# Performance work log

Measured on AMD Instinct MI355X. Metric: run time of the kernel, lower is better.

The kernel has to match this reference:

```python
import jax, jax.numpy as jnp
import numpy as np

N, IN_DIM, NUM_HEADS, HEAD_DIM = 8192, 256, 4, 64
NEG_SLOPE = 0.2


def setup_inputs() -> dict:
    key = jax.random.key(0)
    k1, k2, k3, k4 = jax.random.split(key, 4)
    h = jax.random.normal(k1, (N, IN_DIM), dtype=jnp.float32)
    adj = jax.random.randint(k2, (N, N), 0, 2, dtype=jnp.int32)
    # xavier-ish init scale for the per-head projection weights and attention vector
    W = jax.random.normal(k3, (NUM_HEADS, IN_DIM, HEAD_DIM), dtype=jnp.float32) * (1.0 / np.sqrt(IN_DIM))
    a = jax.random.normal(k4, (2 * HEAD_DIM, 1), dtype=jnp.float32) * (1.0 / np.sqrt(2 * HEAD_DIM))
    return {"h": h, "adj": adj, "W": W, "a": a}


def reference(h, adj, W, a):
    # Wh: (H, N, D) -- per-head linear projection (no bias)
    Wh = jnp.einsum('ni,hid->hnd', h, W)
    # torch computes cat([Wh_i, Wh_j]) @ a; equivalent decomposition:
    # e_ij = (Wh_i . a[:D]) + (Wh_j . a[D:])  -- avoids the O(N^2 * 2D) concat tensor
    a1 = a[:HEAD_DIM, 0]  # (D,)
    a2 = a[HEAD_DIM:, 0]  # (D,)
    s_i = jnp.einsum('hnd,d->hn', Wh, a1)  # (H, N)
    s_j = jnp.einsum('hnd,d->hn', Wh, a2)  # (H, N)
    e = s_i[:, :, None] + s_j[:, None, :]  # (H, N, N)
    e = jnp.where(e > 0, e, NEG_SLOPE * e)  # leaky_relu(0.2)
    e = jnp.where(adj[None, :, :] == 0, -jnp.inf, e)
    att = jax.nn.softmax(e, axis=-1)  # torch softmax(dim=1) over last axis of (N,N)
    # dropout is identity in eval mode
    out = jnp.einsum('hnm,hmd->hnd', att, Wh)  # (H, N, D)
    # concat head outputs along feature dim -> (N, H*D)
    return jnp.transpose(out, (1, 0, 2)).reshape(N, NUM_HEADS * HEAD_DIM)
```

## Files before the change

### kernel.cpp

```cpp
#include <hip/hip_runtime.h>
#include <hip/hip_bf16.h>

#define NND 8192

typedef __attribute__((ext_vector_type(8))) __bf16 bf16x8;
typedef __attribute__((ext_vector_type(4))) float f32x4;
typedef __attribute__((ext_vector_type(4))) unsigned int u32x4;
typedef __attribute__((ext_vector_type(4))) int i32x4;

__global__ __launch_bounds__(256) void gat_phase1(
    const float* __restrict__ hin, const float* __restrict__ W, const float* __restrict__ av,
    float* __restrict__ s1, float* __restrict__ s2, unsigned short* __restrict__ whbT)
{
  const int t = threadIdx.x;
  const int head = t >> 6, lane = t & 63;
  const int lo = lane & 15, kg = lane >> 4;
  const int n0 = blockIdx.x * 16;
  const float* hrow = hin + (size_t)(n0 + lo) * 256;
  const float* Wp = W + head * 16384;
  f32x4 acc[4];
  #pragma unroll
  for (int rt = 0; rt < 4; ++rt) acc[rt] = (f32x4)(0.f);

  #pragma unroll 2
  for (int ks = 0; ks < 8; ++ks) {
    const int kb = ks * 32 + kg * 8;
    f32x4 h0 = *(const f32x4*)(hrow + kb);
    f32x4 h1 = *(const f32x4*)(hrow + kb + 4);
    bf16x8 bf;
    #pragma unroll
    for (int e = 0; e < 4; ++e) { bf[e] = (__bf16)h0[e]; bf[e + 4] = (__bf16)h1[e]; }
    #pragma unroll
    for (int rt = 0; rt < 4; ++rt) {
      bf16x8 af;
      #pragma unroll
      for (int e = 0; e < 8; ++e)
        af[e] = (__bf16)Wp[(kb + e) * 64 + rt * 16 + lo];
      acc[rt] = __builtin_amdgcn_mfma_f32_16x16x32_bf16(af, bf, acc[rt], 0, 0, 0);
    }
  }
  #pragma unroll
  for (int rt = 0; rt < 4; ++rt) {
    #pragma unroll
    for (int r = 0; r < 4; ++r) {
      int hd = head * 64 + rt * 16 + kg * 4 + r;
      whbT[(size_t)hd * NND + n0 + lo] =
          __builtin_bit_cast(unsigned short, (__bf16)acc[rt][r]);
    }
  }
  float p1 = 0.f, p2 = 0.f;
  #pragma unroll
  for (int rt = 0; rt < 4; ++rt) {
    #pragma unroll
    for (int r = 0; r < 4; ++r) {
      int d = rt * 16 + kg * 4 + r;
      p1 = __builtin_fmaf(acc[rt][r], av[d], p1);
      p2 = __builtin_fmaf(acc[rt][r], av[64 + d], p2);
    }
  }
  p1 += __shfl_xor(p1, 16, 64); p1 += __shfl_xor(p1, 32, 64);
  p2 += __shfl_xor(p2, 16, 64); p2 += __shfl_xor(p2, 32, 64);
  if (kg == 0) {
    s1[head * NND + n0 + lo] = p1;
    s2[head * NND + n0 + lo] = p2;
  }
}

__global__ __launch_bounds__(1024, 4) void gat_phase2(
    const int* __restrict__ adj, const float* __restrict__ s1, const float* __restrict__ s2,
    const unsigned short* __restrict__ whbT, float* __restrict__ out)
{
  __shared__ float red[4][64][36];
  const int t = threadIdx.x;
  const int wave = t >> 6, lane = t & 63;
  const int head = wave & 3, jseg = wave >> 2;
  const int i0 = blockIdx.x * 32;
  const int lo = lane & 15, kg = lane >> 4;
  const float s1v0 = s1[head * NND + i0 + lo];
  const float s1v1 = s1[head * NND + i0 + 16 + lo];
  const float* s2h = s2 + head * NND;
  const unsigned short* wb0 = whbT + (size_t)(head * 64 + lo) * NND;
  const unsigned short* wb1 = wb0 + (size_t)16 * NND;
  const unsigned short* wb2 = wb0 + (size_t)32 * NND;
  const unsigned short* wb3 = wb0 + (size_t)48 * NND;
  const int* adjR0 = adj + (size_t)(i0 + lo) * NND;
  const int* adjR1 = adj + (size_t)(i0 + 16 + lo) * NND;
  f32x4 acc0[4], acc1[4];
  #pragma unroll
  for (int dt = 0; dt < 4; ++dt) { acc0[dt] = (f32x4)(0.f); acc1[dt] = (f32x4)(0.f); }
  float den0 = 0.f, den1 = 0.f;
  const int jbase = jseg * 2048;

  for (int jt = 0; jt < 32; ++jt) {
    const int j0 = jbase + jt * 64;
    #pragma unroll
    for (int ks = 0; ks < 2; ++ks) {
      const int jb = j0 + ks * 32 + kg * 8;
      u32x4 b0 = *(const u32x4*)(wb0 + jb);
      u32x4 b1 = *(const u32x4*)(wb1 + jb);
      u32x4 b2 = *(const u32x4*)(wb2 + jb);
      u32x4 b3 = *(const u32x4*)(wb3 + jb);
      i32x4 m0a = *(const i32x4*)(adjR0 + jb);
      i32x4 m0b = *(const i32x4*)(adjR0 + jb + 4);
      i32x4 m1a = *(const i32x4*)(adjR1 + jb);
      i32x4 m1b = *(const i32x4*)(adjR1 + jb + 4);
      f32x4 sa = *(const f32x4*)(s2h + jb);
      f32x4 sb = *(const f32x4*)(s2h + jb + 4);
      {
        bf16x8 af;
        #pragma unroll
        for (int e = 0; e < 4; ++e) {
          float x = s1v0 + sa[e];
          x = fmaxf(x, 0.2f * x);
          float w = (m0a[e] != 0) ? __expf(x) : 0.0f;
          af[e] = (__bf16)w;
          den0 += (float)af[e];
        }
        #pragma unroll
        for (int e = 0; e < 4; ++e) {
          float x = s1v0 + sb[e];
          x = fmaxf(x, 0.2f * x);
          float w = (m0b[e] != 0) ? __expf(x) : 0.0f;
          af[e + 4] = (__bf16)w;
          den0 += (float)af[e + 4];
        }
        acc0[0] = __builtin_amdgcn_mfma_f32_16x16x32_bf16(af, __builtin_bit_cast(bf16x8, b0), acc0[0], 0, 0, 0);
        acc0[1] = __builtin_amdgcn_mfma_f32_16x16x32_bf16(af, __builtin_bit_cast(bf16x8, b1), acc0[1], 0, 0, 0);
        acc0[2] = __builtin_amdgcn_mfma_f32_16x16x32_bf16(af, __builtin_bit_cast(bf16x8, b2), acc0[2], 0, 0, 0);
        acc0[3] = __builtin_amdgcn_mfma_f32_16x16x32_bf16(af, __builtin_bit_cast(bf16x8, b3), acc0[3], 0, 0, 0);
      }
      {
        bf16x8 af;
        #pragma unroll
        for (int e = 0; e < 4; ++e) {
          float x = s1v1 + sa[e];
          x = fmaxf(x, 0.2f * x);
          float w = (m1a[e] != 0) ? __expf(x) : 0.0f;
          af[e] = (__bf16)w;
          den1 += (float)af[e];
        }
        #pragma unroll
        for (int e = 0; e < 4; ++e) {
          float x = s1v1 + sb[e];
          x = fmaxf(x, 0.2f * x);
          float w = (m1b[e] != 0) ? __expf(x) : 0.0f;
          af[e + 4] = (__bf16)w;
          den1 += (float)af[e + 4];
        }
        acc1[0] = __builtin_amdgcn_mfma_f32_16x16x32_bf16(af, __builtin_bit_cast(bf16x8, b0), acc1[0], 0, 0, 0);
        acc1[1] = __builtin_amdgcn_mfma_f32_16x16x32_bf16(af, __builtin_bit_cast(bf16x8, b1), acc1[1], 0, 0, 0);
        acc1[2] = __builtin_amdgcn_mfma_f32_16x16x32_bf16(af, __builtin_bit_cast(bf16x8, b2), acc1[2], 0, 0, 0);
        acc1[3] = __builtin_amdgcn_mfma_f32_16x16x32_bf16(af, __builtin_bit_cast(bf16x8, b3), acc1[3], 0, 0, 0);
      }
    }
  }
  den0 += __shfl_xor(den0, 16, 64); den0 += __shfl_xor(den0, 32, 64);
  den1 += __shfl_xor(den1, 16, 64); den1 += __shfl_xor(den1, 32, 64);

  for (int s = 1; s <= 3; ++s) {
    if (jseg == s) {
      #pragma unroll
      for (int dt = 0; dt < 4; ++dt) {
        *(f32x4*)&red[head][lane][dt * 4]      = acc0[dt];
        *(f32x4*)&red[head][lane][16 + dt * 4] = acc1[dt];
      }
      red[head][lane][32] = den0;
      red[head][lane][33] = den1;
    }
    __syncthreads();
    if (jseg == 0) {
      #pragma unroll
      for (int dt = 0; dt < 4; ++dt) {
        acc0[dt] += *(const f32x4*)&red[head][lane][dt * 4];
        acc1[dt] += *(const f32x4*)&red[head][lane][16 + dt * 4];
      }
      den0 += red[head][lane][32];
      den1 += red[head][lane][33];
    }
    __syncthreads();
  }
  if (jseg != 0) return;

  #pragma unroll
  for (int r = 0; r < 4; ++r) {
    float dr0 = __shfl(den0, kg * 4 + r, 64);
    float dr1 = __shfl(den1, kg * 4 + r, 64);
    float rc0 = 1.0f / dr0, rc1 = 1.0f / dr1;
    float* op0 = out + (size_t)(i0 + kg * 4 + r) * 256 + head * 64 + lo;
    float* op1 = out + (size_t)(i0 + 16 + kg * 4 + r) * 256 + head * 64 + lo;
    #pragma unroll
    for (int dt = 0; dt < 4; ++dt) {
      op0[dt * 16] = acc0[dt][r] * rc0;
      op1[dt * 16] = acc1[dt][r] * rc1;
    }
  }
}

extern "C" void kernel_launch(void* const* d_in, const int* in_sizes, int n_in,
                              void* d_out, int out_size, void* d_ws, size_t ws_size,
                              hipStream_t stream) {
  const float* h   = (const float*)d_in[0];
  const int*   adj = (const int*)d_in[1];
  const float* W   = (const float*)d_in[2];
  const float* a   = (const float*)d_in[3];
  float* out = (float*)d_out;
  float* s1 = (float*)d_ws;
  float* s2 = s1 + 4 * NND;
  unsigned short* whbT = (unsigned short*)(s2 + 4 * NND);
  gat_phase1<<<dim3(NND / 16), dim3(256), 0, stream>>>(h, W, a, s1, s2, whbT);
  gat_phase2<<<dim3(NND / 32), dim3(1024), 0, stream>>>(adj, s1, s2, whbT, out);
}
```

Baseline: 568.0 us.

## Bit-pack adjacency, prefragment Wh layout, fold attention vector into W, MFMA denominators

```diff
diff --git a/kernel.cpp b/kernel.cpp
--- a/kernel.cpp
+++ b/kernel.cpp
@@ -6,71 +6,111 @@
 typedef __attribute__((ext_vector_type(8))) __bf16 bf16x8;
 typedef __attribute__((ext_vector_type(4))) float f32x4;
 typedef __attribute__((ext_vector_type(4))) unsigned int u32x4;
-typedef __attribute__((ext_vector_type(4))) int i32x4;
-
-__global__ __launch_bounds__(256) void gat_phase1(
-    const float* __restrict__ hin, const float* __restrict__ W, const float* __restrict__ av,
-    float* __restrict__ s1, float* __restrict__ s2, unsigned short* __restrict__ whbT)
+typedef __attribute__((ext_vector_type(2))) unsigned int u32x2;
+
+__global__ __launch_bounds__(256) void gat_phase0(
+    const int* __restrict__ adj, unsigned long long* __restrict__ bits)
+{
+  const int wave = threadIdx.x >> 6, lane = threadIdx.x & 63;
+  const int row = blockIdx.x * 4 + wave;
+  const int* ap = adj + (size_t)row * NND + lane;
+  unsigned long long* bp = bits + (size_t)row * 128;
+  #pragma unroll 4
+  for (int it = 0; it < 128; ++it) {
+    int v = ap[it * 64];
+    unsigned long long m = __ballot(v != 0);
+    if (lane == 0) bp[it] = m;
+  }
+}
+
+__global__ __launch_bounds__(256) void gat_phase1a(
+    const float* __restrict__ W, const float* __restrict__ av,
+    float* __restrict__ q1, float* __restrict__ q2)
+{
+  const int t = blockIdx.x * 256 + threadIdx.x;
+  const float* wp = W + (size_t)t * 64;
+  float p1 = 0.f, p2 = 0.f;
+  #pragma unroll
+  for (int d = 0; d < 64; d += 4) {
+    f32x4 w  = *(const f32x4*)(wp + d);
+    f32x4 a1 = *(const f32x4*)(av + d);
+    f32x4 a2 = *(const f32x4*)(av + 64 + d);
+    p1 += w[0]*a1[0] + w[1]*a1[1] + w[2]*a1[2] + w[3]*a1[3];
+    p2 += w[0]*a2[0] + w[1]*a2[1] + w[2]*a2[2] + w[3]*a2[3];
+  }
+  q1[t] = p1 * 1.4426950408889634f;
+  q2[t] = p2 * 1.4426950408889634f;
+}
+
+__global__ __launch_bounds__(1024) void gat_phase1(
+    const float* __restrict__ hin, const float* __restrict__ W,
+    const float* __restrict__ q1, const float* __restrict__ q2,
+    float* __restrict__ s1, float* __restrict__ s2, unsigned int* __restrict__ whbF)
 {
   const int t = threadIdx.x;
-  const int head = t >> 6, lane = t & 63;
+  const int wave = t >> 6, lane = t & 63;
+  const int head = wave & 3, dt = wave >> 2;
   const int lo = lane & 15, kg = lane >> 4;
-  const int n0 = blockIdx.x * 16;
-  const float* hrow = hin + (size_t)(n0 + lo) * 256;
-  const float* Wp = W + head * 16384;
-  f32x4 acc[4];
-  #pragma unroll
-  for (int rt = 0; rt < 4; ++rt) acc[rt] = (f32x4)(0.f);
-
-  #pragma unroll 2
-  for (int ks = 0; ks < 8; ++ks) {
-    const int kb = ks * 32 + kg * 8;
-    f32x4 h0 = *(const f32x4*)(hrow + kb);
-    f32x4 h1 = *(const f32x4*)(hrow + kb + 4);
-    bf16x8 bf;
-    #pragma unroll
-    for (int e = 0; e < 4; ++e) { bf[e] = (__bf16)h0[e]; bf[e + 4] = (__bf16)h1[e]; }
-    #pragma unroll
-    for (int rt = 0; rt < 4; ++rt) {
-      bf16x8 af;
-      #pragma unroll
-      for (int e = 0; e < 8; ++e)
-        af[e] = (__bf16)Wp[(kb + e) * 64 + rt * 16 + lo];
-      acc[rt] = __builtin_amdgcn_mfma_f32_16x16x32_bf16(af, bf, acc[rt], 0, 0, 0);
-    }
-  }
-  #pragma unroll
-  for (int rt = 0; rt < 4; ++rt) {
-    #pragma unroll
-    for (int r = 0; r < 4; ++r) {
-      int hd = head * 64 + rt * 16 + kg * 4 + r;
-      whbT[(size_t)hd * NND + n0 + lo] =
-          __builtin_bit_cast(unsigned short, (__bf16)acc[rt][r]);
-    }
-  }
-  float p1 = 0.f, p2 = 0.f;
-  #pragma unroll
-  for (int rt = 0; rt < 4; ++rt) {
-    #pragma unroll
-    for (int r = 0; r < 4; ++r) {
-      int d = rt * 16 + kg * 4 + r;
-      p1 = __builtin_fmaf(acc[rt][r], av[d], p1);
-      p2 = __builtin_fmaf(acc[rt][r], av[64 + d], p2);
-    }
-  }
-  p1 += __shfl_xor(p1, 16, 64); p1 += __shfl_xor(p1, 32, 64);
-  p2 += __shfl_xor(p2, 16, 64); p2 += __shfl_xor(p2, 32, 64);
-  if (kg == 0) {
-    s1[head * NND + n0 + lo] = p1;
-    s2[head * NND + n0 + lo] = p2;
-  }
-}
-
-__global__ __launch_bounds__(1024, 4) void gat_phase2(
-    const int* __restrict__ adj, const float* __restrict__ s1, const float* __restrict__ s2,
-    const unsigned short* __restrict__ whbT, float* __restrict__ out)
-{
-  __shared__ float red[4][64][36];
+  const float* Wp = W + head * 16384 + dt * 16 + lo;
+  bf16x8 wf[8];
+  #pragma unroll
+  for (int ks = 0; ks < 8; ++ks)
+    #pragma unroll
+    for (int e = 0; e < 8; ++e)
+      wf[ks][e] = (__bf16)Wp[(ks * 32 + kg * 8 + e) * 64];
+  const float* q1h = q1 + head * 256;
+  const float* q2h = q2 + head * 256;
+
+  #pragma unroll
+  for (int c = 0; c < 2; ++c) {
+    const int n0 = blockIdx.x * 32 + c * 16;
+    const float* hrow = hin + (size_t)(n0 + lo) * 256;
+    f32x4 acc = (f32x4)(0.f);
+    float p1 = 0.f, p2 = 0.f;
+    #pragma unroll
+    for (int ks = 0; ks < 8; ++ks) {
+      const int kb = ks * 32 + kg * 8;
+      f32x4 h0 = *(const f32x4*)(hrow + kb);
+      f32x4 h1 = *(const f32x4*)(hrow + kb + 4);
+      bf16x8 hf;
+      #pragma unroll
+      for (int e = 0; e < 4; ++e) { hf[e] = (__bf16)h0[e]; hf[e + 4] = (__bf16)h1[e]; }
+      acc = __builtin_amdgcn_mfma_f32_16x16x32_bf16(hf, wf[ks], acc, 0, 0, 0);
+      if (dt == 0) {
+        f32x4 qa = *(const f32x4*)(q1h + kb);
+        f32x4 qb = *(const f32x4*)(q1h + kb + 4);
+        f32x4 qc = *(const f32x4*)(q2h + kb);
+        f32x4 qd = *(const f32x4*)(q2h + kb + 4);
+        #pragma unroll
+        for (int e = 0; e < 4; ++e) {
+          p1 = fmaf(h0[e], qa[e], p1); p1 = fmaf(h1[e], qb[e], p1);
+          p2 = fmaf(h0[e], qc[e], p2); p2 = fmaf(h1[e], qd[e], p2);
+        }
+      }
+    }
+    const int jtg = n0 >> 6, sub = (n0 >> 4) & 3;
+    const int chunk = ((head * 4 + dt) * 128 + jtg) * 2 + (kg >> 1);
+    unsigned short b0 = __builtin_bit_cast(unsigned short, (__bf16)acc[0]);
+    unsigned short b1 = __builtin_bit_cast(unsigned short, (__bf16)acc[1]);
+    unsigned short b2 = __builtin_bit_cast(unsigned short, (__bf16)acc[2]);
+    unsigned short b3 = __builtin_bit_cast(unsigned short, (__bf16)acc[3]);
+    u32x2 wv; wv[0] = (unsigned)b0 | ((unsigned)b1 << 16);
+    wv[1] = (unsigned)b2 | ((unsigned)b3 << 16);
+    *(u32x2*)(whbF + (size_t)chunk * 256 + (sub * 16 + lo) * 4 + (kg & 1) * 2) = wv;
+    if (dt == 0) {
+      p1 += __shfl_xor(p1, 16, 64); p1 += __shfl_xor(p1, 32, 64);
+      p2 += __shfl_xor(p2, 16, 64); p2 += __shfl_xor(p2, 32, 64);
+      if (kg == 0) { s1[head * NND + n0 + lo] = p1; s2[head * NND + n0 + lo] = p2; }
+    }
+  }
+}
+
+__global__ __launch_bounds__(1024) void gat_phase2(
+    const unsigned long long* __restrict__ bits, const float* __restrict__ s1,
+    const float* __restrict__ s2, const unsigned short* __restrict__ whbF,
+    float* __restrict__ out)
+{
+  __shared__ float red[4][64][44];
   const int t = threadIdx.x;
   const int wave = t >> 6, lane = t & 63;
   const int head = wave & 3, jseg = wave >> 2;
@@ -78,94 +118,93 @@
   const int lo = lane & 15, kg = lane >> 4;
   const float s1v0 = s1[head * NND + i0 + lo];
   const float s1v1 = s1[head * NND + i0 + 16 + lo];
+  const unsigned char* br0 = (const unsigned char*)bits + (size_t)(i0 + lo) * 1024 + kg * 2;
+  const unsigned char* br1 = br0 + 16 * 1024;
   const float* s2h = s2 + head * NND;
-  const unsigned short* wb0 = whbT + (size_t)(head * 64 + lo) * NND;
-  const unsigned short* wb1 = wb0 + (size_t)16 * NND;
-  const unsigned short* wb2 = wb0 + (size_t)32 * NND;
-  const unsigned short* wb3 = wb0 + (size_t)48 * NND;
-  const int* adjR0 = adj + (size_t)(i0 + lo) * NND;
-  const int* adjR1 = adj + (size_t)(i0 + 16 + lo) * NND;
-  f32x4 acc0[4], acc1[4];
+  const char* wfb = (const char*)whbF + (size_t)head * 1048576 + (size_t)lane * 16;
+  f32x4 acc0[4], acc1[4], dn0 = (f32x4)(0.f), dn1 = (f32x4)(0.f);
   #pragma unroll
   for (int dt = 0; dt < 4; ++dt) { acc0[dt] = (f32x4)(0.f); acc1[dt] = (f32x4)(0.f); }
-  float den0 = 0.f, den1 = 0.f;
-  const int jbase = jseg * 2048;
-
+  bf16x8 ones;
+  #pragma unroll
+  for (int e = 0; e < 8; ++e) ones[e] = (__bf16)1.0f;
+
+  auto mkaf = [&](float s1v, unsigned m, f32x4 sa, f32x4 sb, int bb) -> bf16x8 {
+    bf16x8 af;
+    #pragma unroll
+    for (int e = 0; e < 4; ++e) {
+      float x = s1v + sa[e];
+      x = fmaxf(x, 0.2f * x);
+      float w = __builtin_amdgcn_exp2f(x);
+      w = ((m >> (bb + e)) & 1u) ? w : 0.0f;
+      af[e] = (__bf16)w;
+    }
+    #pragma unroll
+    for (int e = 0; e < 4; ++e) {
+      float x = s1v + sb[e];
+      x = fmaxf(x, 0.2f * x);
+      float w = __builtin_amdgcn_exp2f(x);
+      w = ((m >> (bb + 4 + e)) & 1u) ? w : 0.0f;
+      af[e + 4] = (__bf16)w;
+    }
+    return af;
+  };
+
+  #pragma unroll 2
   for (int jt = 0; jt < 32; ++jt) {
-    const int j0 = jbase + jt * 64;
-    #pragma unroll
-    for (int ks = 0; ks < 2; ++ks) {
-      const int jb = j0 + ks * 32 + kg * 8;
-      u32x4 b0 = *(const u32x4*)(wb0 + jb);
-      u32x4 b1 = *(const u32x4*)(wb1 + jb);
-      u32x4 b2 = *(const u32x4*)(wb2 + jb);
-      u32x4 b3 = *(const u32x4*)(wb3 + jb);
-      i32x4 m0a = *(const i32x4*)(adjR0 + jb);
-      i32x4 m0b = *(const i32x4*)(adjR0 + jb + 4);
-      i32x4 m1a = *(const i32x4*)(adjR1 + jb);
-      i32x4 m1b = *(const i32x4*)(adjR1 + jb + 4);
-      f32x4 sa = *(const f32x4*)(s2h + jb);
-      f32x4 sb = *(const f32x4*)(s2h + jb + 4);
-      {
-        bf16x8 af;
-        #pragma unroll
-        for (int e = 0; e < 4; ++e) {
-          float x = s1v0 + sa[e];
-          x = fmaxf(x, 0.2f * x);
-          float w = (m0a[e] != 0) ? __expf(x) : 0.0f;
-          af[e] = (__bf16)w;
-          den0 += (float)af[e];
-        }
-        #pragma unroll
-        for (int e = 0; e < 4; ++e) {
-          float x = s1v0 + sb[e];
-          x = fmaxf(x, 0.2f * x);
-          float w = (m0b[e] != 0) ? __expf(x) : 0.0f;
-          af[e + 4] = (__bf16)w;
-          den0 += (float)af[e + 4];
-        }
-        acc0[0] = __builtin_amdgcn_mfma_f32_16x16x32_bf16(af, __builtin_bit_cast(bf16x8, b0), acc0[0], 0, 0, 0);
-        acc0[1] = __builtin_amdgcn_mfma_f32_16x16x32_bf16(af, __builtin_bit_cast(bf16x8, b1), acc0[1], 0, 0, 0);
-        acc0[2] = __builtin_amdgcn_mfma_f32_16x16x32_bf16(af, __builtin_bit_cast(bf16x8, b2), acc0[2], 0, 0, 0);
-        acc0[3] = __builtin_amdgcn_mfma_f32_16x16x32_bf16(af, __builtin_bit_cast(bf16x8, b3), acc0[3], 0, 0, 0);
-      }
-      {
-        bf16x8 af;
-        #pragma unroll
-        for (int e = 0; e < 4; ++e) {
-          float x = s1v1 + sa[e];
-          x = fmaxf(x, 0.2f * x);
-          float w = (m1a[e] != 0) ? __expf(x) : 0.0f;
-          af[e] = (__bf16)w;
-          den1 += (float)af[e];
-        }
-        #pragma unroll
-        for (int e = 0; e < 4; ++e) {
-          float x = s1v1 + sb[e];
-          x = fmaxf(x, 0.2f * x);
-          float w = (m1b[e] != 0) ? __expf(x) : 0.0f;
-          af[e + 4] = (__bf16)w;
-          den1 += (float)af[e + 4];
-        }
-        acc1[0] = __builtin_amdgcn_mfma_f32_16x16x32_bf16(af, __builtin_bit_cast(bf16x8, b0), acc1[0], 0, 0, 0);
-        acc1[1] = __builtin_amdgcn_mfma_f32_16x16x32_bf16(af, __builtin_bit_cast(bf16x8, b1), acc1[1], 0, 0, 0);
-        acc1[2] = __builtin_amdgcn_mfma_f32_16x16x32_bf16(af, __builtin_bit_cast(bf16x8, b2), acc1[2], 0, 0, 0);
-        acc1[3] = __builtin_amdgcn_mfma_f32_16x16x32_bf16(af, __builtin_bit_cast(bf16x8, b3), acc1[3], 0, 0, 0);
-      }
-    }
-  }
-  den0 += __shfl_xor(den0, 16, 64); den0 += __shfl_xor(den0, 32, 64);
-  den1 += __shfl_xor(den1, 16, 64); den1 += __shfl_xor(den1, 32, 64);
+    const int jtg = jseg * 32 + jt;
+    const int j0 = jtg * 64;
+    u32x4 bb[8];
+    #pragma unroll
+    for (int dt = 0; dt < 4; ++dt)
+      #pragma unroll
+      for (int ks = 0; ks < 2; ++ks)
+        bb[dt * 2 + ks] = *(const u32x4*)(wfb + dt * 262144 + jtg * 2048 + ks * 1024);
+    const unsigned m0 = *(const unsigned short*)(br0 + (j0 >> 3));
+    const unsigned m1 = *(const unsigned short*)(br1 + (j0 >> 3));
+    const f32x4 sv0 = *(const f32x4*)(s2h + j0 + kg * 16);
+    const f32x4 sv1 = *(const f32x4*)(s2h + j0 + kg * 16 + 4);
+    const f32x4 sv2 = *(const f32x4*)(s2h + j0 + kg * 16 + 8);
+    const f32x4 sv3 = *(const f32x4*)(s2h + j0 + kg * 16 + 12);
+    {
+      bf16x8 af = mkaf(s1v0, m0, sv0, sv1, 0);
+      acc0[0] = __builtin_amdgcn_mfma_f32_16x16x32_bf16(af, __builtin_bit_cast(bf16x8, bb[0]), acc0[0], 0, 0, 0);
+      acc0[1] = __builtin_amdgcn_mfma_f32_16x16x32_bf16(af, __builtin_bit_cast(bf16x8, bb[2]), acc0[1], 0, 0, 0);
+      acc0[2] = __builtin_amdgcn_mfma_f32_16x16x32_bf16(af, __builtin_bit_cast(bf16x8, bb[4]), acc0[2], 0, 0, 0);
+      acc0[3] = __builtin_amdgcn_mfma_f32_16x16x32_bf16(af, __builtin_bit_cast(bf16x8, bb[6]), acc0[3], 0, 0, 0);
+      dn0 = __builtin_amdgcn_mfma_f32_16x16x32_bf16(af, ones, dn0, 0, 0, 0);
+      af = mkaf(s1v0, m0, sv2, sv3, 8);
+      acc0[0] = __builtin_amdgcn_mfma_f32_16x16x32_bf16(af, __builtin_bit_cast(bf16x8, bb[1]), acc0[0], 0, 0, 0);
+      acc0[1] = __builtin_amdgcn_mfma_f32_16x16x32_bf16(af, __builtin_bit_cast(bf16x8, bb[3]), acc0[1], 0, 0, 0);
+      acc0[2] = __builtin_amdgcn_mfma_f32_16x16x32_bf16(af, __builtin_bit_cast(bf16x8, bb[5]), acc0[2], 0, 0, 0);
+      acc0[3] = __builtin_amdgcn_mfma_f32_16x16x32_bf16(af, __builtin_bit_cast(bf16x8, bb[7]), acc0[3], 0, 0, 0);
+      dn0 = __builtin_amdgcn_mfma_f32_16x16x32_bf16(af, ones, dn0, 0, 0, 0);
+    }
+    {
+      bf16x8 af = mkaf(s1v1, m1, sv0, sv1, 0);
+      acc1[0] = __builtin_amdgcn_mfma_f32_16x16x32_bf16(af, __builtin_bit_cast(bf16x8, bb[0]), acc1[0], 0, 0, 0);
+      acc1[1] = __builtin_amdgcn_mfma_f32_16x16x32_bf16(af, __builtin_bit_cast(bf16x8, bb[2]), acc1[1], 0, 0, 0);
+      acc1[2] = __builtin_amdgcn_mfma_f32_16x16x32_bf16(af, __builtin_bit_cast(bf16x8, bb[4]), acc1[2], 0, 0, 0);
+      acc1[3] = __builtin_amdgcn_mfma_f32_16x16x32_bf16(af, __builtin_bit_cast(bf16x8, bb[6]), acc1[3], 0, 0, 0);
+      dn1 = __builtin_amdgcn_mfma_f32_16x16x32_bf16(af, ones, dn1, 0, 0, 0);
+      af = mkaf(s1v1, m1, sv2, sv3, 8);
+      acc1[0] = __builtin_amdgcn_mfma_f32_16x16x32_bf16(af, __builtin_bit_cast(bf16x8, bb[1]), acc1[0], 0, 0, 0);
+      acc1[1] = __builtin_amdgcn_mfma_f32_16x16x32_bf16(af, __builtin_bit_cast(bf16x8, bb[3]), acc1[1], 0, 0, 0);
+      acc1[2] = __builtin_amdgcn_mfma_f32_16x16x32_bf16(af, __builtin_bit_cast(bf16x8, bb[5]), acc1[2], 0, 0, 0);
+      acc1[3] = __builtin_amdgcn_mfma_f32_16x16x32_bf16(af, __builtin_bit_cast(bf16x8, bb[7]), acc1[3], 0, 0, 0);
+      dn1 = __builtin_amdgcn_mfma_f32_16x16x32_bf16(af, ones, dn1, 0, 0, 0);
+    }
+  }
 
   for (int s = 1; s <= 3; ++s) {
     if (jseg == s) {
       #pragma unroll
       for (int dt = 0; dt < 4; ++dt) {
-        *(f32x4*)&red[head][lane][dt * 4]      = acc0[dt];
+        *(f32x4*)&red[head][lane][dt * 4] = acc0[dt];
         *(f32x4*)&red[head][lane][16 + dt * 4] = acc1[dt];
       }
-      red[head][lane][32] = den0;
-      red[head][lane][33] = den1;
+      *(f32x4*)&red[head][lane][32] = dn0;
+      *(f32x4*)&red[head][lane][36] = dn1;
     }
     __syncthreads();
     if (jseg == 0) {
@@ -174,8 +213,8 @@
         acc0[dt] += *(const f32x4*)&red[head][lane][dt * 4];
         acc1[dt] += *(const f32x4*)&red[head][lane][16 + dt * 4];
       }
-      den0 += red[head][lane][32];
-      den1 += red[head][lane][33];
+      dn0 += *(const f32x4*)&red[head][lane][32];
+      dn1 += *(const f32x4*)&red[head][lane][36];
     }
     __syncthreads();
   }
@@ -183,11 +222,9 @@
 
   #pragma unroll
   for (int r = 0; r < 4; ++r) {
-    float dr0 = __shfl(den0, kg * 4 + r, 64);
-    float dr1 = __shfl(den1, kg * 4 + r, 64);
-    float rc0 = 1.0f / dr0, rc1 = 1.0f / dr1;
+    const float rc0 = 1.0f / dn0[r], rc1 = 1.0f / dn1[r];
     float* op0 = out + (size_t)(i0 + kg * 4 + r) * 256 + head * 64 + lo;
-    float* op1 = out + (size_t)(i0 + 16 + kg * 4 + r) * 256 + head * 64 + lo;
+    float* op1 = op0 + 16 * 256;
     #pragma unroll
     for (int dt = 0; dt < 4; ++dt) {
       op0[dt * 16] = acc0[dt][r] * rc0;
@@ -206,7 +243,12 @@
   float* out = (float*)d_out;
   float* s1 = (float*)d_ws;
   float* s2 = s1 + 4 * NND;
-  unsigned short* whbT = (unsigned short*)(s2 + 4 * NND);
-  gat_phase1<<<dim3(NND / 16), dim3(256), 0, stream>>>(h, W, a, s1, s2, whbT);
-  gat_phase2<<<dim3(NND / 32), dim3(1024), 0, stream>>>(adj, s1, s2, whbT, out);
-}
+  float* q1 = s2 + 4 * NND;
+  float* q2 = q1 + 1024;
+  unsigned long long* bits = (unsigned long long*)(q2 + 1024);
+  unsigned int* whbF = (unsigned int*)(bits + (size_t)NND * 128);
+  gat_phase0<<<dim3(NND / 4), dim3(256), 0, stream>>>(adj, bits);
+  gat_phase1a<<<dim3(4), dim3(256), 0, stream>>>(W, a, q1, q2);
+  gat_phase1<<<dim3(NND / 32), dim3(1024), 0, stream>>>(h, W, q1, q2, s1, s2, whbF);
+  gat_phase2<<<dim3(NND / 32), dim3(1024), 0, stream>>>(bits, s1, s2, (const unsigned short*)whbF, out);
+}
```

Result: no change. 564.4 us (-0.6%).
